# Optimization experiments

Hardware: AMD Instinct MI355X
Metric: run time of the kernel (lower is better)

The kernel has to match this reference:

```python
import jax, jax.numpy as jnp
import numpy as np

S, D, H, HD = 3072, 1280, 16, 80
FF = 4 * D
EPS = 1e-6


def layernorm(x, scale, bias):
    mu = jnp.mean(x, axis=-1, keepdims=True)
    var = jnp.mean(jnp.square(x - mu), axis=-1, keepdims=True)
    return (x - mu) * jax.lax.rsqrt(var + EPS) * scale + bias


def rotate_half(x):
    x1 = x[..., : x.shape[-1] // 2]
    x2 = x[..., x.shape[-1] // 2 :]
    return jnp.concatenate([-x2, x1], axis=-1)


def apply_rope(x, freqs):
    # x: (S,H,hd), freqs: (S,hd/2)
    cos = jnp.repeat(jnp.cos(freqs), 2, axis=-1)[:, None, :]  # (S,1,hd)
    sin = jnp.repeat(jnp.sin(freqs), 2, axis=-1)[:, None, :]
    return x * cos + rotate_half(x) * sin


def quick_gelu(x):
    return x * jax.nn.sigmoid(1.702 * x)


def setup_inputs() -> dict:
    key = jax.random.key(0)
    ks = jax.random.split(key, 12)
    s = 0.02
    return {
        "hidden_states": jax.random.normal(ks[0], (S, D), jnp.float32),
        "rotary_pos_emb": jax.random.normal(ks[1], (S, HD // 2), jnp.float32),
        "ln1_scale": jnp.ones((D,), jnp.float32),
        "ln1_bias": jnp.zeros((D,), jnp.float32),
        "ln2_scale": jnp.ones((D,), jnp.float32),
        "ln2_bias": jnp.zeros((D,), jnp.float32),
        "qkv_w": jax.random.normal(ks[2], (D, 3 * D), jnp.float32) * s,
        "qkv_b": jnp.zeros((3 * D,), jnp.float32),
        "proj_w": jax.random.normal(ks[3], (D, D), jnp.float32) * s,
        "proj_b": jnp.zeros((D,), jnp.float32),
        "fc1_w": jax.random.normal(ks[4], (D, FF), jnp.float32) * s,
        "fc1_b": jnp.zeros((FF,), jnp.float32),
        "fc2_w": jax.random.normal(ks[5], (FF, D), jnp.float32) * s,
        "fc2_b": jnp.zeros((D,), jnp.float32),
        "cu_seqlens": jnp.array([0, 1024, 2048, 3072], jnp.int32),
    }


def reference(hidden_states, rotary_pos_emb, ln1_scale, ln1_bias, ln2_scale,
              ln2_bias, qkv_w, qkv_b, proj_w, proj_b, fc1_w, fc1_b, fc2_w,
              fc2_b, cu_seqlens):
    x = hidden_states  # (S, D)
    h = layernorm(x, ln1_scale, ln1_bias)
    qkv = (h @ qkv_w + qkv_b).reshape(S, 3, H, HD)
    q, k, v = qkv[:, 0], qkv[:, 1], qkv[:, 2]  # each (S, H, hd)
    q = apply_rope(q, rotary_pos_emb)
    k = apply_rope(k, rotary_pos_emb)

    # block-diagonal varlen mask from cu_seqlens (same segment attends)
    ids = jnp.arange(S)
    seg = jnp.searchsorted(cu_seqlens, ids, side="right")  # (S,)
    valid = seg[:, None] == seg[None, :]  # (S, S)
    bias = jnp.where(valid, 0.0, jnp.finfo(q.dtype).min)

    scale = 1.0 / jnp.sqrt(jnp.asarray(HD, q.dtype))
    scores = jnp.einsum("qhd,khd->hqk", q, k) * scale + bias
    probs = jax.nn.softmax(scores.astype(jnp.float32), axis=-1).astype(q.dtype)
    attn = jnp.einsum("hqk,khd->qhd", probs, v).reshape(S, D)
    attn = attn @ proj_w + proj_b

    x = x + attn
    h2 = layernorm(x, ln2_scale, ln2_bias)
    mlp = quick_gelu(h2 @ fc1_w + fc1_b) @ fc2_w + fc2_b
    return x + mlp
```

## Files before the change

### kernel.cpp

```cpp
#include <hip/hip_runtime.h>

typedef __bf16 bf16x8 __attribute__((ext_vector_type(8)));
typedef float f32x4 __attribute__((ext_vector_type(4)));
typedef unsigned short u16;
typedef u16 u16x2 __attribute__((ext_vector_type(2)));
typedef u16 u16x4 __attribute__((ext_vector_type(4)));
typedef u16 u16x8 __attribute__((ext_vector_type(8)));
typedef float float4v __attribute__((ext_vector_type(4)));

__device__ __forceinline__ u16 f2bf(float f) {
    __bf16 b = (__bf16)f;
    return __builtin_bit_cast(unsigned short, b);
}
__device__ __forceinline__ float bf2f(u16 x) {
    __bf16 b = __builtin_bit_cast(__bf16, x);
    return (float)b;
}

__device__ __forceinline__ void gld16(const void* g, void* l) {
    __builtin_amdgcn_global_load_lds((const __attribute__((address_space(1))) void*)g,
                                     (__attribute__((address_space(3))) void*)l, 16, 0, 0);
}

__device__ __forceinline__ int xcd_swz(int orig, int nwg) {
    const int q = nwg >> 3, r = nwg & 7;
    const int xcd = orig & 7, pos = orig >> 3;
    return (xcd < r ? xcd * (q + 1) : r * (q + 1) + (xcd - r) * q) + pos;
}

__global__ __launch_bounds__(256) void transpose_all_kernel(
    const float* __restrict__ qkvw, const float* __restrict__ projw,
    const float* __restrict__ fc1w, const float* __restrict__ fc2w,
    u16* __restrict__ qkvwT, u16* __restrict__ projwT,
    u16* __restrict__ fc1wT, u16* __restrict__ fc2wT)
{
    __shared__ u16 tile[64][65];
    int bid = blockIdx.x;
    const float* W; u16* WT; int K, N, nx;
    if (bid < 1200)      { W = qkvw;  WT = qkvwT;  K = 1280; N = 3840; nx = 60; }
    else if (bid < 1600) { bid -= 1200; W = projw; WT = projwT; K = 1280; N = 1280; nx = 20; }
    else if (bid < 3200) { bid -= 1600; W = fc1w;  WT = fc1wT;  K = 1280; N = 5120; nx = 80; }
    else                 { bid -= 3200; W = fc2w;  WT = fc2wT;  K = 5120; N = 1280; nx = 20; }
    const int tx = threadIdx.x & 63, ty = threadIdx.x >> 6;
    const int n0 = (bid % nx) * 64, k0 = (bid / nx) * 64;
    #pragma unroll
    for (int i = ty; i < 64; i += 4)
        tile[i][tx] = f2bf(W[(size_t)(k0 + i) * N + n0 + tx]);
    __syncthreads();
    const int txh = threadIdx.x & 31, tyh = threadIdx.x >> 5;
    #pragma unroll
    for (int i = tyh; i < 64; i += 8) {
        u16x2 v2;
        v2[0] = tile[2 * txh][i];
        v2[1] = tile[2 * txh + 1][i];
        *reinterpret_cast<u16x2*>(&WT[(size_t)(n0 + i) * K + k0 + 2 * txh]) = v2;
    }
}

__global__ __launch_bounds__(256) void vtrans_kernel(
    const u16* __restrict__ qkv, u16* __restrict__ vt)
{
    __shared__ u16 tile[64][65];
    const int bs = blockIdx.x % 48, bd = blockIdx.x / 48;
    const int s0 = bs * 64, d0 = bd * 64;
    const int tx = threadIdx.x & 63, ty = threadIdx.x >> 6;
    #pragma unroll
    for (int i = ty; i < 64; i += 4)
        tile[i][tx] = qkv[(size_t)(s0 + i) * 3840 + 2560 + d0 + tx];
    __syncthreads();
    const int txh = threadIdx.x & 31, tyh = threadIdx.x >> 5;
    #pragma unroll
    for (int i = tyh; i < 64; i += 8) {
        u16x2 v2;
        v2[0] = tile[2 * txh][i];
        v2[1] = tile[2 * txh + 1][i];
        *reinterpret_cast<u16x2*>(&vt[(size_t)(d0 + i) * 3072 + s0 + 2 * txh]) = v2;
    }
}

__global__ __launch_bounds__(256) void ln_kernel(
    const float* __restrict__ x, const float* __restrict__ sc,
    const float* __restrict__ bias, u16* __restrict__ out)
{
    const int row = blockIdx.x, t = threadIdx.x;
    const float* xr = x + (size_t)row * 1280;
    float v[5], s1 = 0.f, s2 = 0.f;
    #pragma unroll
    for (int i = 0; i < 5; i++) {
        v[i] = xr[t + i * 256];
        s1 += v[i];
        s2 += v[i] * v[i];
    }
    #pragma unroll
    for (int off = 32; off; off >>= 1) {
        s1 += __shfl_down(s1, off);
        s2 += __shfl_down(s2, off);
    }
    __shared__ float rA[4], rB[4];
    if ((t & 63) == 0) { rA[t >> 6] = s1; rB[t >> 6] = s2; }
    __syncthreads();
    s1 = rA[0] + rA[1] + rA[2] + rA[3];
    s2 = rB[0] + rB[1] + rB[2] + rB[3];
    const float mu = s1 * (1.f / 1280.f);
    const float var = s2 * (1.f / 1280.f) - mu * mu;
    const float rstd = rsqrtf(var + 1e-6f);
    #pragma unroll
    for (int i = 0; i < 5; i++) {
        const int d = t + i * 256;
        out[(size_t)row * 1280 + d] = f2bf((v[i] - mu) * rstd * sc[d] + bias[d]);
    }
}

__global__ __launch_bounds__(256) void reduce4_ln_kernel(
    const u16* __restrict__ parts, const float* __restrict__ bias,
    const float* __restrict__ res, const float* __restrict__ lns,
    const float* __restrict__ lnb, float* __restrict__ xmid,
    u16* __restrict__ h2, size_t MN)
{
    const int row = blockIdx.x, t = threadIdx.x;
    float v[5], s1 = 0.f, s2 = 0.f;
    #pragma unroll
    for (int i = 0; i < 5; i++) {
        const int d = t + i * 256;
        const size_t idx = (size_t)row * 1280 + d;
        float a = bf2f(parts[idx]) + bf2f(parts[MN + idx])
                + bf2f(parts[2 * MN + idx]) + bf2f(parts[3 * MN + idx])
                + res[idx] + bias[d];
        v[i] = a;
        xmid[idx] = a;
        s1 += a;
        s2 += a * a;
    }
    #pragma unroll
    for (int off = 32; off; off >>= 1) {
        s1 += __shfl_down(s1, off);
        s2 += __shfl_down(s2, off);
    }
    __shared__ float rA[4], rB[4];
    if ((t & 63) == 0) { rA[t >> 6] = s1; rB[t >> 6] = s2; }
    __syncthreads();
    s1 = rA[0] + rA[1] + rA[2] + rA[3];
    s2 = rB[0] + rB[1] + rB[2] + rB[3];
    const float mu = s1 * (1.f / 1280.f);
    const float var = s2 * (1.f / 1280.f) - mu * mu;
    const float rstd = rsqrtf(var + 1e-6f);
    #pragma unroll
    for (int i = 0; i < 5; i++) {
        const int d = t + i * 256;
        h2[(size_t)row * 1280 + d] = f2bf((v[i] - mu) * rstd * lns[d] + lnb[d]);
    }
}

__global__ __launch_bounds__(256) void reduce4b_kernel(
    const u16* __restrict__ parts, const float* __restrict__ bias,
    const float* __restrict__ res, float* __restrict__ out, int N, size_t MN)
{
    const size_t i4 = ((size_t)blockIdx.x * 256 + threadIdx.x) * 4;
    if (i4 >= MN) return;
    float4v a = *reinterpret_cast<const float4v*>(res + i4);
    #pragma unroll
    for (int p = 0; p < 4; p++) {
        u16x4 v = *reinterpret_cast<const u16x4*>(parts + p * MN + i4);
        #pragma unroll
        for (int r = 0; r < 4; r++) a[r] += bf2f(v[r]);
    }
    const int col = (int)(i4 % N);
    a += *reinterpret_cast<const float4v*>(bias + col);
    *reinterpret_cast<float4v*>(out + i4) = a;
}

template <int GELU, int OUTB, int SPLIT>
__global__ __launch_bounds__(512, 2) void gemm256_kernel(
    const u16* __restrict__ A, const u16* __restrict__ BT,
    const float* __restrict__ bias,
    float* __restrict__ outF, u16* __restrict__ outB,
    int M, int N, int K)
{
    __shared__ u16 As[2][256 * 64];
    __shared__ u16 Bs[2][256 * 64];
    const int tid = threadIdx.x, lane = tid & 63, wave = tid >> 6;
    const int nwg = gridDim.x * gridDim.y;
    const int bid = xcd_swz(blockIdx.y * gridDim.x + blockIdx.x, nwg);
    const int m0 = (bid / gridDim.x) * 256, n0 = (bid % gridDim.x) * 256;
    const int wr = wave >> 2, wc = wave & 3;
    const int wm = wr * 128, wn = wc * 64;
    const int lr = lane & 15, lh = lane >> 4;
    const int xa = lr & 7;

    const int kchunk = K / SPLIT;
    const int kz = (SPLIT > 1) ? blockIdx.z : 0;
    const int kbeg = kz * kchunk;
    const int niter = kchunk >> 7;

    const int sr = lane >> 3;
    const int sc8 = (lane & 7) ^ sr;

    f32x4 acc[8][4] = {};
    bf16x8 bq[4][2];

    const char* aRd[2] = {
        (const char*)As + (wm + lr) * 128 + ((0 + lh) ^ xa) * 16,
        (const char*)As + (wm + lr) * 128 + ((4 + lh) ^ xa) * 16 };
    const char* bRd[2] = {
        (const char*)Bs + (wn + lr) * 128 + ((0 + lh) ^ xa) * 16,
        (const char*)Bs + (wn + lr) * 128 + ((4 + lh) ^ xa) * 16 };

    const u16 *aG[2][2], *bG[2][2];
    #pragma unroll
    for (int h = 0; h < 2; h++)
        #pragma unroll
        for (int j = 0; j < 2; j++) {
            const int row = h * 128 + j * 64 + wave * 8 + sr;
            aG[h][j] = A + (size_t)(m0 + row) * K + kbeg + sc8 * 8;
            bG[h][j] = BT + (size_t)(n0 + row) * K + kbeg + sc8 * 8;
        }

    auto stgA = [&](int t, int h) {
        u16* d = (u16*)As + (t & 1) * 16384 + h * 8192 + wave * 512;
        gld16(aG[h][0] + (size_t)t * 64, d);
        gld16(aG[h][1] + (size_t)t * 64, d + 4096);
    };
    auto stgB = [&](int t, int h) {
        u16* d = (u16*)Bs + (t & 1) * 16384 + h * 8192 + wave * 512;
        gld16(bG[h][0] + (size_t)t * 64, d);
        gld16(bG[h][1] + (size_t)t * 64, d + 4096);
    };

#define PHASE(BUF, Q, STGSTMT, WAITSTMT)                                        \
    {                                                                           \
        if ((Q) == 0) {                                                         \
            _Pragma("unroll") for (int ni = 0; ni < 4; ni++)                    \
                _Pragma("unroll") for (int kk = 0; kk < 2; kk++)                \
                    bq[ni][kk] = *reinterpret_cast<const bf16x8*>(              \
                        bRd[kk] + (BUF) * 32768 + ni * 2048);                   \
        }                                                                       \
        bf16x8 afq[2][2];                                                       \
        _Pragma("unroll") for (int m2 = 0; m2 < 2; m2++)                        \
            _Pragma("unroll") for (int kk = 0; kk < 2; kk++)                    \
                afq[m2][kk] = *reinterpret_cast<const bf16x8*>(                 \
                    aRd[kk] + (BUF) * 32768 + (Q) * 4096 + m2 * 2048);          \
        STGSTMT;                                                                \
        __builtin_amdgcn_s_barrier();                                           \
        asm volatile("s_waitcnt lgkmcnt(0)" ::: "memory");                      \
        __builtin_amdgcn_s_setprio(1);                                          \
        _Pragma("unroll") for (int kk = 0; kk < 2; kk++)                        \
            _Pragma("unroll") for (int m2 = 0; m2 < 2; m2++)                    \
                _Pragma("unroll") for (int ni = 0; ni < 4; ni++)                \
                    acc[(Q) * 2 + m2][ni] =                                     \
                        __builtin_amdgcn_mfma_f32_16x16x32_bf16(                \
                            afq[m2][kk], bq[ni][kk], acc[(Q) * 2 + m2][ni],     \
                            0, 0, 0);                                           \
        __builtin_amdgcn_s_setprio(0);                                          \
        WAITSTMT;                                                               \
        __builtin_amdgcn_s_barrier();                                           \
    }

    stgB(0, 0); stgB(0, 1);
    stgA(0, 0); stgA(0, 1);
    stgB(1, 0); stgB(1, 1);
    asm volatile("s_waitcnt vmcnt(4)" ::: "memory");
    __builtin_amdgcn_s_barrier();

    for (int i = 0; i < niter - 1; i++) {
        const int t0 = 2 * i, t1 = 2 * i + 1;
        PHASE(0, 0, stgA(t1, 0), (void)0);
        PHASE(0, 1, stgA(t1, 1), (void)0);
        PHASE(0, 2, stgB(t0 + 2, 0), (void)0);
        PHASE(0, 3, stgB(t0 + 2, 1),
              asm volatile("s_waitcnt vmcnt(4)" ::: "memory"));
        PHASE(1, 0, stgA(t0 + 2, 0), (void)0);
        PHASE(1, 1, stgA(t0 + 2, 1), (void)0);
        PHASE(1, 2, stgB(t1 + 2, 0), (void)0);
        PHASE(1, 3, stgB(t1 + 2, 1),
              asm volatile("s_waitcnt vmcnt(4)" ::: "memory"));
    }
    {
        const int t1 = 2 * niter - 1;
        PHASE(0, 0, stgA(t1, 0), (void)0);
        PHASE(0, 1, stgA(t1, 1), (void)0);
        PHASE(0, 2, (void)0, (void)0);
        PHASE(0, 3, (void)0,
              asm volatile("s_waitcnt vmcnt(0)" ::: "memory"));
        PHASE(1, 0, (void)0, (void)0);
        PHASE(1, 1, (void)0, (void)0);
        PHASE(1, 2, (void)0, (void)0);
        PHASE(1, 3, (void)0, (void)0);
    }
#undef PHASE

    if (SPLIT > 1) {
        u16* pf = outB + (size_t)kz * M * N;
        #pragma unroll
        for (int mi = 0; mi < 8; mi++)
            #pragma unroll
            for (int ni = 0; ni < 4; ni++) {
                const int col = n0 + wn + ni * 16 + lr;
                #pragma unroll
                for (int r = 0; r < 4; r++) {
                    const int rowg = m0 + wm + mi * 16 + lh * 4 + r;
                    pf[(size_t)rowg * N + col] = f2bf(acc[mi][ni][r]);
                }
            }
        return;
    }

    #pragma unroll
    for (int mi = 0; mi < 8; mi++) {
        #pragma unroll
        for (int ni = 0; ni < 4; ni++) {
            const int col = n0 + wn + ni * 16 + lr;
            const float bv = bias[col];
            #pragma unroll
            for (int r = 0; r < 4; r++) {
                const int rowg = m0 + wm + mi * 16 + lh * 4 + r;
                float v = acc[mi][ni][r] + bv;
                if (GELU) v = v * (1.0f / (1.0f + __expf(-1.702f * v)));
                if (OUTB) outB[(size_t)rowg * N + col] = f2bf(v);
            }
        }
    }
}

template <int SPLIT>
__global__ __launch_bounds__(256) void gemm_kernel(
    const u16* __restrict__ A, const u16* __restrict__ BT,
    u16* __restrict__ partB, int M, int N, int K)
{
    __shared__ u16 As[128 * 64];
    __shared__ u16 Bs[128 * 64];
    const int tid = threadIdx.x, lane = tid & 63, wave = tid >> 6;
    const int nwg = gridDim.x * gridDim.y;
    const int bid = xcd_swz(blockIdx.y * gridDim.x + blockIdx.x, nwg);
    const int m0 = (bid / gridDim.x) * 128, n0 = (bid % gridDim.x) * 128;
    const int wm = (wave >> 1) * 64, wn = (wave & 1) * 64;
    const int lr = lane & 15, lh = lane >> 4;
    const int xa = lr & 7;
    const int srow = lane >> 3;
    const int schunk = (lane & 7) ^ (srow & 7);

    const int kchunk = K / SPLIT;
    const int kz = (SPLIT > 1) ? blockIdx.z : 0;
    const int kbeg = kz * kchunk;

    const u16 *aG[4], *bG[4];
    u16 *dA[4], *dB[4];
    #pragma unroll
    for (int s = 0; s < 4; s++) {
        const int seg = wave + s * 4;
        const int row = seg * 8 + srow;
        aG[s] = A + (size_t)(m0 + row) * K + kbeg + schunk * 8;
        bG[s] = BT + (size_t)(n0 + row) * K + kbeg + schunk * 8;
        dA[s] = As + seg * 512;
        dB[s] = Bs + seg * 512;
    }
    const char* aRd[2] = {
        (const char*)As + (wm + lr) * 128 + ((0 + lh) ^ xa) * 16,
        (const char*)As + (wm + lr) * 128 + ((4 + lh) ^ xa) * 16 };
    const char* bRd[2] = {
        (const char*)Bs + (wn + lr) * 128 + ((0 + lh) ^ xa) * 16,
        (const char*)Bs + (wn + lr) * 128 + ((4 + lh) ^ xa) * 16 };

    f32x4 acc[4][4] = {};

    for (int ko = 0; ko < kchunk; ko += 64) {
        #pragma unroll
        for (int s = 0; s < 4; s++) {
            gld16(aG[s] + ko, dA[s]);
            gld16(bG[s] + ko, dB[s]);
        }
        asm volatile("s_waitcnt vmcnt(0)" ::: "memory");
        __syncthreads();

        bf16x8 af[4][2], bfr[4][2];
        #pragma unroll
        for (int mi = 0; mi < 4; mi++)
            #pragma unroll
            for (int kk = 0; kk < 2; kk++)
                af[mi][kk] = *reinterpret_cast<const bf16x8*>(aRd[kk] + mi * 2048);
        #pragma unroll
        for (int ni = 0; ni < 4; ni++)
            #pragma unroll
            for (int kk = 0; kk < 2; kk++)
                bfr[ni][kk] = *reinterpret_cast<const bf16x8*>(bRd[kk] + ni * 2048);
        #pragma unroll
        for (int kk = 0; kk < 2; kk++)
            #pragma unroll
            for (int mi = 0; mi < 4; mi++)
                #pragma unroll
                for (int ni = 0; ni < 4; ni++)
                    acc[mi][ni] = __builtin_amdgcn_mfma_f32_16x16x32_bf16(
                        af[mi][kk], bfr[ni][kk], acc[mi][ni], 0, 0, 0);
        __syncthreads();
    }

    u16* pf = partB + (size_t)kz * M * N;
    #pragma unroll
    for (int mi = 0; mi < 4; mi++)
        #pragma unroll
        for (int ni = 0; ni < 4; ni++) {
            const int col = n0 + wn + ni * 16 + lr;
            #pragma unroll
            for (int r = 0; r < 4; r++) {
                const int rowg = m0 + wm + mi * 16 + lh * 4 + r;
                pf[(size_t)rowg * N + col] = f2bf(acc[mi][ni][r]);
            }
        }
}

__global__ __launch_bounds__(256) void rope_kernel(
    const u16* __restrict__ qkv, const float* __restrict__ freqs,
    u16* __restrict__ qp, u16* __restrict__ kp)
{
    const int s = blockIdx.x, t = threadIdx.x;
    const float scale = 0.1118033988749895f;
    __shared__ float cs[40], sn[40];
    if (t < 40) {
        const float f = freqs[(size_t)s * 40 + t];
        cs[t] = cosf(f);
        sn[t] = sinf(f);
    }
    __syncthreads();
    const u16* row = qkv + (size_t)s * 3840;
    for (int i = t; i < 1280; i += 256) {
        const int h = i / 80, d = i % 80;
        const float c = cs[d >> 1], sv = sn[d >> 1];
        const float q0 = bf2f(row[i]);
        const float q1 = (d < 40) ? -bf2f(row[i + 40]) : bf2f(row[i - 40]);
        qp[((size_t)h * 3072 + s) * 96 + d] = f2bf((q0 * c + q1 * sv) * scale);
        const float k0 = bf2f(row[1280 + i]);
        const float k1 = (d < 40) ? -bf2f(row[1280 + i + 40]) : bf2f(row[1280 + i - 40]);
        kp[((size_t)h * 3072 + s) * 128 + d] = f2bf(k0 * c + k1 * sv);
    }
    {
        const int h = t / 16, d = 80 + (t % 16);
        qp[((size_t)h * 3072 + s) * 96 + d] = 0;
    }
    for (int i = t; i < 768; i += 256) {
        const int h = i / 48, d = 80 + (i % 48);
        kp[((size_t)h * 3072 + s) * 128 + d] = 0;
    }
}

__global__ __launch_bounds__(256) void attn_kernel(
    const u16* __restrict__ qp, const u16* __restrict__ kp,
    const u16* __restrict__ vt, u16* __restrict__ attn_out)
{
    const int tid = threadIdx.x, lane = tid & 63, wave = tid >> 6;
    const int w = xcd_swz(blockIdx.x, 768);
    const int qt = w & 15;
    const int h = (w >> 4) & 15;
    const int sq = w >> 8;
    const int lr = lane & 15, lh = lane >> 4;
    const int xa = lr & 7;
    const int qrow = sq * 1024 + qt * 64 + wave * 16;

    __shared__ u16 Ks[2][64 * 128];
    __shared__ u16 Vs[2][80 * 64];

    bf16x8 aq[3];
    {
        const u16* qb = qp + ((size_t)h * 3072 + qrow + lr) * 96 + lh * 8;
        #pragma unroll
        for (int d0 = 0; d0 < 3; d0++)
            aq[d0] = *reinterpret_cast<const bf16x8*>(qb + d0 * 32);
    }

    float m = -1e30f, l = 0.f;
    f32x4 acc[5] = {};

    const u16* kseg = kp + ((size_t)h * 3072 + sq * 1024) * 128;
    const u16* vseg = vt + (size_t)h * 80 * 3072 + sq * 1024;

    const int krow_l = lane >> 4;
    const int kch    = lane & 15;
    const int vrow_l = lane >> 3;
    const int vch    = lane & 7;

    const u16 *kG[4], *vG[3];
    u16 *kD[4], *vD[3];
    #pragma unroll
    for (int s = 0; s < 4; s++) {
        const int seg = wave + s * 4;
        const int row = seg * 4 + krow_l;
        kG[s] = kseg + (size_t)row * 128 + ((kch ^ (row & 7)) * 8);
        kD[s] = (u16*)Ks + seg * 512;
    }
    #pragma unroll
    for (int s = 0; s < 3; s++) {
        const int seg = wave + s * 4;
        const int row = (seg < 10) ? seg * 8 + vrow_l : 0;
        vG[s] = vseg + (size_t)row * 3072 + ((vch ^ (row & 7)) * 8);
        vD[s] = (u16*)Vs + seg * 512;
    }

    auto stageK = [&](int t, int buf) {
        #pragma unroll
        for (int s = 0; s < 4; s++)
            gld16(kG[s] + (size_t)t * 8192, kD[s] + buf * 8192);
    };
    auto stageV = [&](int t, int buf) {
        #pragma unroll
        for (int s = 0; s < 3; s++)
            if (wave + s * 4 < 10)
                gld16(vG[s] + t * 64, vD[s] + buf * 5120);
    };

    stageK(0, 0);
    stageV(0, 0);
    asm volatile("s_waitcnt vmcnt(0)" ::: "memory");
    __syncthreads();

    const char* kRd[3] = {
        (const char*)Ks + lr * 256 + ((0 + lh) ^ xa) * 16,
        (const char*)Ks + lr * 256 + ((4 + lh) ^ xa) * 16,
        (const char*)Ks + lr * 256 + ((8 + lh) ^ xa) * 16 };
    const char* vRd[2] = {
        (const char*)Vs + lr * 128 + ((0 + lh) ^ xa) * 16,
        (const char*)Vs + lr * 128 + ((4 + lh) ^ xa) * 16 };

    const int prow = wave * 16 + lr;
    const int psw = prow & 7;
    const char* pBase = (const char*)Ks + prow * 256;
    const int prd = ((12 + lh) ^ psw) << 4;

    for (int t = 0; t < 16; t++) {
        const int cur = t & 1;
        const int curK = cur * 16384, curV = cur * 10240;
        if (t < 15) {
            stageK(t + 1, cur ^ 1);
            stageV(t + 1, cur ^ 1);
        }

        f32x4 sc[4] = {};
        #pragma unroll
        for (int c = 0; c < 4; c++) {
            #pragma unroll
            for (int d0 = 0; d0 < 3; d0++) {
                bf16x8 kf = *reinterpret_cast<const bf16x8*>(kRd[d0] + curK + c * 4096);
                sc[c] = __builtin_amdgcn_mfma_f32_16x16x32_bf16(kf, aq[d0], sc[c], 0, 0, 0);
            }
        }

        float pmax = sc[0][0];
        #pragma unroll
        for (int c = 0; c < 4; c++)
            #pragma unroll
            for (int r = 0; r < 4; r++)
                pmax = fmaxf(pmax, sc[c][r]);
        pmax = fmaxf(pmax, __shfl_xor(pmax, 16));
        pmax = fmaxf(pmax, __shfl_xor(pmax, 32));

        if (!__all(pmax - m <= 8.0f)) {
            const float mn = fmaxf(m, pmax);
            const float fac = __expf(m - mn);
            m = mn;
            l *= fac;
            #pragma unroll
            for (int df = 0; df < 5; df++)
                #pragma unroll
                for (int r = 0; r < 4; r++)
                    acc[df][r] *= fac;
        }

        float p[4][4], rs = 0.f;
        #pragma unroll
        for (int c = 0; c < 4; c++)
            #pragma unroll
            for (int r = 0; r < 4; r++) {
                p[c][r] = __expf(sc[c][r] - m);
                rs += p[c][r];
            }
        rs += __shfl_xor(rs, 16);
        rs += __shfl_xor(rs, 32);
        l += rs;

        char* pb = (char*)pBase + curK;

        #pragma unroll
        for (int cc = 0; cc < 2; cc++) {
            u16x4 pw;
            #pragma unroll
            for (int r = 0; r < 4; r++)
                pw[r] = f2bf(p[cc][r]);
            *reinterpret_cast<u16x4*>(
                pb + (((12 + cc * 2 + (lh >> 1)) ^ psw) << 4) + (lh & 1) * 8) = pw;
        }
        asm volatile("s_waitcnt lgkmcnt(0)" ::: "memory");
        {
            bf16x8 pa = *reinterpret_cast<const bf16x8*>(pb + prd);
            asm volatile("s_waitcnt lgkmcnt(0)" ::: "memory");
            #pragma unroll
            for (int df = 0; df < 5; df++) {
                bf16x8 vf = *reinterpret_cast<const bf16x8*>(vRd[0] + curV + df * 2048);
                acc[df] = __builtin_amdgcn_mfma_f32_16x16x32_bf16(vf, pa, acc[df], 0, 0, 0);
            }
        }
        #pragma unroll
        for (int cc = 0; cc < 2; cc++) {
            u16x4 pw;
            #pragma unroll
            for (int r = 0; r < 4; r++)
                pw[r] = f2bf(p[2 + cc][r]);
            *reinterpret_cast<u16x4*>(
                pb + (((12 + cc * 2 + (lh >> 1)) ^ psw) << 4) + (lh & 1) * 8) = pw;
        }
        asm volatile("s_waitcnt lgkmcnt(0)" ::: "memory");
        {
            bf16x8 pa = *reinterpret_cast<const bf16x8*>(pb + prd);
            #pragma unroll
            for (int df = 0; df < 5; df++) {
                bf16x8 vf = *reinterpret_cast<const bf16x8*>(vRd[1] + curV + df * 2048);
                acc[df] = __builtin_amdgcn_mfma_f32_16x16x32_bf16(vf, pa, acc[df], 0, 0, 0);
            }
        }

        asm volatile("s_waitcnt vmcnt(0)" ::: "memory");
        __syncthreads();
    }

    const float invl = 1.0f / l;
    u16* orow = attn_out + (size_t)(qrow + lr) * 1280 + h * 80;
    #pragma unroll
    for (int df = 0; df < 5; df++) {
        u16x4 o;
        #pragma unroll
        for (int r = 0; r < 4; r++)
            o[r] = f2bf(acc[df][r] * invl);
        *reinterpret_cast<u16x4*>(orow + df * 16 + lh * 4) = o;
    }
}

extern "C" void kernel_launch(void* const* d_in, const int* in_sizes, int n_in,
                              void* d_out, int out_size, void* d_ws, size_t ws_size,
                              hipStream_t stream) {
    const float* hidden = (const float*)d_in[0];
    const float* rot    = (const float*)d_in[1];
    const float* ln1s   = (const float*)d_in[2];
    const float* ln1b   = (const float*)d_in[3];
    const float* ln2s   = (const float*)d_in[4];
    const float* ln2b   = (const float*)d_in[5];
    const float* qkvw   = (const float*)d_in[6];
    const float* qkvb   = (const float*)d_in[7];
    const float* projw  = (const float*)d_in[8];
    const float* projb  = (const float*)d_in[9];
    const float* fc1w   = (const float*)d_in[10];
    const float* fc1b   = (const float*)d_in[11];
    const float* fc2w   = (const float*)d_in[12];
    const float* fc2b   = (const float*)d_in[13];
    float* out = (float*)d_out;

    char* p = (char*)d_ws;
    auto alloc = [&](size_t n) { char* r = p; p += (n + 255) & ~(size_t)255; return r; };
    u16* qkvwT  = (u16*)alloc((size_t)3840 * 1280 * 2);
    u16* projwT = (u16*)alloc((size_t)1280 * 1280 * 2);
    u16* fc1wT  = (u16*)alloc((size_t)5120 * 1280 * 2);
    u16* fc2wT  = (u16*)alloc((size_t)1280 * 5120 * 2);
    u16* hbuf   = (u16*)alloc((size_t)3072 * 1280 * 2);
    u16* qkvbf  = (u16*)alloc((size_t)3072 * 5120 * 2);
    u16* attnb  = (u16*)alloc((size_t)3072 * 1280 * 2);
    float* xmid = (float*)alloc((size_t)3072 * 1280 * 4);
    u16* partsB = (u16*)alloc((size_t)4 * 3072 * 1280 * 2);
    u16* qp2 = partsB;
    u16* kp2 = qp2 + (size_t)16 * 3072 * 96;
    u16* vt2 = kp2 + (size_t)16 * 3072 * 128;
    u16* h2   = hbuf;
    u16* mlp1 = qkvbf;
    const size_t MN = (size_t)3072 * 1280;

    transpose_all_kernel<<<4800, 256, 0, stream>>>(
        qkvw, projw, fc1w, fc2w, qkvwT, projwT, fc1wT, fc2wT);

    ln_kernel<<<3072, 256, 0, stream>>>(hidden, ln1s, ln1b, hbuf);
    gemm256_kernel<0, 1, 1><<<dim3(15, 12), 512, 0, stream>>>(
        hbuf, qkvwT, qkvb, nullptr, qkvbf, 3072, 3840, 1280);
    rope_kernel<<<3072, 256, 0, stream>>>(qkvbf, rot, qp2, kp2);
    vtrans_kernel<<<960, 256, 0, stream>>>(qkvbf, vt2);
    attn_kernel<<<768, 256, 0, stream>>>(qp2, kp2, vt2, attnb);
    gemm_kernel<4><<<dim3(10, 24, 4), 256, 0, stream>>>(
        attnb, projwT, partsB, 3072, 1280, 1280);
    reduce4_ln_kernel<<<3072, 256, 0, stream>>>(
        partsB, projb, hidden, ln2s, ln2b, xmid, h2, MN);
    gemm256_kernel<1, 1, 1><<<dim3(20, 12), 512, 0, stream>>>(
        h2, fc1wT, fc1b, nullptr, mlp1, 3072, 5120, 1280);
    gemm256_kernel<0, 0, 4><<<dim3(5, 12, 4), 512, 0, stream>>>(
        mlp1, fc2wT, fc2b, nullptr, partsB, 3072, 1280, 5120);
    reduce4b_kernel<<<(int)(MN / 4 / 256), 256, 0, stream>>>(partsB, fc2b, xmid, out, 1280, MN);
}
```

Before: 263.2 us.

## Triple-buffer A tiles in gemm256 and store mid residual as bf16

The 256x256 GEMM now keeps three LDS buffers for A and two for B, with a rotating buffer schedule that prefetches two K-tiles ahead. It also replaces the runtime iteration count with a fully scheduled 20-tile loop, which assumes K equals 1280. The aim is to hide more global-load latency behind MFMA work, but the larger LDS footprint (160 KB) likely prevents two blocks per CU and lowers occupancy. Separately, the post-attention residual xmid is stored in bf16 instead of fp32 to cut memory traffic in the reduce kernels, at some cost in accuracy of the residual path.

Measured after the change: 266.1 us. No clear change (+1.1%).

```diff
diff --git a/kernel.cpp b/kernel.cpp
--- a/kernel.cpp
+++ b/kernel.cpp
@@ -114,7 +114,7 @@
 __global__ __launch_bounds__(256) void reduce4_ln_kernel(
     const u16* __restrict__ parts, const float* __restrict__ bias,
     const float* __restrict__ res, const float* __restrict__ lns,
-    const float* __restrict__ lnb, float* __restrict__ xmid,
+    const float* __restrict__ lnb, u16* __restrict__ xmid,
     u16* __restrict__ h2, size_t MN)
 {
     const int row = blockIdx.x, t = threadIdx.x;
@@ -127,7 +127,7 @@
                 + bf2f(parts[2 * MN + idx]) + bf2f(parts[3 * MN + idx])
                 + res[idx] + bias[d];
         v[i] = a;
-        xmid[idx] = a;
+        xmid[idx] = f2bf(a);
         s1 += a;
         s2 += a * a;
     }
@@ -153,11 +153,14 @@
 
 __global__ __launch_bounds__(256) void reduce4b_kernel(
     const u16* __restrict__ parts, const float* __restrict__ bias,
-    const float* __restrict__ res, float* __restrict__ out, int N, size_t MN)
+    const u16* __restrict__ res, float* __restrict__ out, int N, size_t MN)
 {
     const size_t i4 = ((size_t)blockIdx.x * 256 + threadIdx.x) * 4;
     if (i4 >= MN) return;
-    float4v a = *reinterpret_cast<const float4v*>(res + i4);
+    float4v a;
+    u16x4 rv = *reinterpret_cast<const u16x4*>(res + i4);
+    #pragma unroll
+    for (int r = 0; r < 4; r++) a[r] = bf2f(rv[r]);
     #pragma unroll
     for (int p = 0; p < 4; p++) {
         u16x4 v = *reinterpret_cast<const u16x4*>(parts + p * MN + i4);
@@ -176,7 +179,7 @@
     float* __restrict__ outF, u16* __restrict__ outB,
     int M, int N, int K)
 {
-    __shared__ u16 As[2][256 * 64];
+    __shared__ u16 As[3][256 * 64];
     __shared__ u16 Bs[2][256 * 64];
     const int tid = threadIdx.x, lane = tid & 63, wave = tid >> 6;
     const int nwg = gridDim.x * gridDim.y;
@@ -190,7 +193,6 @@
     const int kchunk = K / SPLIT;
     const int kz = (SPLIT > 1) ? blockIdx.z : 0;
     const int kbeg = kz * kchunk;
-    const int niter = kchunk >> 7;
 
     const int sr = lane >> 3;
     const int sc8 = (lane & 7) ^ sr;
@@ -198,12 +200,18 @@
     f32x4 acc[8][4] = {};
     bf16x8 bq[4][2];
 
-    const char* aRd[2] = {
-        (const char*)As + (wm + lr) * 128 + ((0 + lh) ^ xa) * 16,
-        (const char*)As + (wm + lr) * 128 + ((4 + lh) ^ xa) * 16 };
-    const char* bRd[2] = {
-        (const char*)Bs + (wn + lr) * 128 + ((0 + lh) ^ xa) * 16,
-        (const char*)Bs + (wn + lr) * 128 + ((4 + lh) ^ xa) * 16 };
+    const char* aRdB[3][2];
+    const char* bRdB[2][2];
+    #pragma unroll
+    for (int b = 0; b < 3; b++)
+        #pragma unroll
+        for (int kk = 0; kk < 2; kk++)
+            aRdB[b][kk] = (const char*)As[b] + (wm + lr) * 128 + ((kk * 4 + lh) ^ xa) * 16;
+    #pragma unroll
+    for (int b = 0; b < 2; b++)
+        #pragma unroll
+        for (int kk = 0; kk < 2; kk++)
+            bRdB[b][kk] = (const char*)Bs[b] + (wn + lr) * 128 + ((kk * 4 + lh) ^ xa) * 16;
 
     const u16 *aG[2][2], *bG[2][2];
     #pragma unroll
@@ -215,30 +223,30 @@
             bG[h][j] = BT + (size_t)(n0 + row) * K + kbeg + sc8 * 8;
         }
 
-    auto stgA = [&](int t, int h) {
-        u16* d = (u16*)As + (t & 1) * 16384 + h * 8192 + wave * 512;
+    auto stgA = [&](int t, int buf, int h) {
+        u16* d = (u16*)As + buf * 16384 + h * 8192 + wave * 512;
         gld16(aG[h][0] + (size_t)t * 64, d);
         gld16(aG[h][1] + (size_t)t * 64, d + 4096);
     };
-    auto stgB = [&](int t, int h) {
-        u16* d = (u16*)Bs + (t & 1) * 16384 + h * 8192 + wave * 512;
+    auto stgB = [&](int t, int buf, int h) {
+        u16* d = (u16*)Bs + buf * 16384 + h * 8192 + wave * 512;
         gld16(bG[h][0] + (size_t)t * 64, d);
         gld16(bG[h][1] + (size_t)t * 64, d + 4096);
     };
 
-#define PHASE(BUF, Q, STGSTMT, WAITSTMT)                                        \
+#define PH3(AB, BB, Q, RDB, STGSTMT, VMSTMT)                                    \
     {                                                                           \
-        if ((Q) == 0) {                                                         \
+        if (RDB) {                                                              \
             _Pragma("unroll") for (int ni = 0; ni < 4; ni++)                    \
                 _Pragma("unroll") for (int kk = 0; kk < 2; kk++)                \
                     bq[ni][kk] = *reinterpret_cast<const bf16x8*>(              \
-                        bRd[kk] + (BUF) * 32768 + ni * 2048);                   \
+                        bRdB[BB][kk] + ni * 2048);                              \
         }                                                                       \
         bf16x8 afq[2][2];                                                       \
         _Pragma("unroll") for (int m2 = 0; m2 < 2; m2++)                        \
             _Pragma("unroll") for (int kk = 0; kk < 2; kk++)                    \
                 afq[m2][kk] = *reinterpret_cast<const bf16x8*>(                 \
-                    aRd[kk] + (BUF) * 32768 + (Q) * 4096 + m2 * 2048);          \
+                    aRdB[AB][kk] + (Q) * 4096 + m2 * 2048);                     \
         STGSTMT;                                                                \
         __builtin_amdgcn_s_barrier();                                           \
         asm volatile("s_waitcnt lgkmcnt(0)" ::: "memory");                      \
@@ -251,42 +259,43 @@
                             afq[m2][kk], bq[ni][kk], acc[(Q) * 2 + m2][ni],     \
                             0, 0, 0);                                           \
         __builtin_amdgcn_s_setprio(0);                                          \
-        WAITSTMT;                                                               \
+        VMSTMT;                                                                 \
         __builtin_amdgcn_s_barrier();                                           \
     }
 
-    stgB(0, 0); stgB(0, 1);
-    stgA(0, 0); stgA(0, 1);
-    stgB(1, 0); stgB(1, 1);
-    asm volatile("s_waitcnt vmcnt(4)" ::: "memory");
+#define ITER3(T, AB, BB, A2)                                                    \
+    PH3(AB, BB, 0, 1, stgA((T) + 2, A2, 0), (void)0);                           \
+    PH3(AB, BB, 1, 0, stgA((T) + 2, A2, 1), (void)0);                           \
+    PH3(AB, BB, 2, 0, stgB((T) + 2, BB, 0), (void)0);                           \
+    PH3(AB, BB, 3, 0, stgB((T) + 2, BB, 1),                                     \
+        asm volatile("s_waitcnt vmcnt(8)" ::: "memory"));
+
+    stgA(0, 0, 0); stgA(0, 0, 1);
+    stgB(0, 0, 0); stgB(0, 0, 1);
+    stgA(1, 1, 0); stgA(1, 1, 1);
+    stgB(1, 1, 0); stgB(1, 1, 1);
+    asm volatile("s_waitcnt vmcnt(8)" ::: "memory");
     __builtin_amdgcn_s_barrier();
 
-    for (int i = 0; i < niter - 1; i++) {
-        const int t0 = 2 * i, t1 = 2 * i + 1;
-        PHASE(0, 0, stgA(t1, 0), (void)0);
-        PHASE(0, 1, stgA(t1, 1), (void)0);
-        PHASE(0, 2, stgB(t0 + 2, 0), (void)0);
-        PHASE(0, 3, stgB(t0 + 2, 1),
-              asm volatile("s_waitcnt vmcnt(4)" ::: "memory"));
-        PHASE(1, 0, stgA(t0 + 2, 0), (void)0);
-        PHASE(1, 1, stgA(t0 + 2, 1), (void)0);
-        PHASE(1, 2, stgB(t1 + 2, 0), (void)0);
-        PHASE(1, 3, stgB(t1 + 2, 1),
-              asm volatile("s_waitcnt vmcnt(4)" ::: "memory"));
-    }
-    {
-        const int t1 = 2 * niter - 1;
-        PHASE(0, 0, stgA(t1, 0), (void)0);
-        PHASE(0, 1, stgA(t1, 1), (void)0);
-        PHASE(0, 2, (void)0, (void)0);
-        PHASE(0, 3, (void)0,
-              asm volatile("s_waitcnt vmcnt(0)" ::: "memory"));
-        PHASE(1, 0, (void)0, (void)0);
-        PHASE(1, 1, (void)0, (void)0);
-        PHASE(1, 2, (void)0, (void)0);
-        PHASE(1, 3, (void)0, (void)0);
-    }
-#undef PHASE
+    for (int tt = 0; tt < 3; tt++) {
+        const int tb = 6 * tt;
+        ITER3(tb + 0, 0, 0, 2);
+        ITER3(tb + 1, 1, 1, 0);
+        ITER3(tb + 2, 2, 0, 1);
+        ITER3(tb + 3, 0, 1, 2);
+        ITER3(tb + 4, 1, 0, 0);
+        ITER3(tb + 5, 2, 1, 1);
+    }
+    PH3(0, 0, 0, 1, (void)0, (void)0);
+    PH3(0, 0, 1, 0, (void)0, (void)0);
+    PH3(0, 0, 2, 0, (void)0, (void)0);
+    PH3(0, 0, 3, 0, (void)0, asm volatile("s_waitcnt vmcnt(0)" ::: "memory"));
+    PH3(1, 1, 0, 1, (void)0, (void)0);
+    PH3(1, 1, 1, 0, (void)0, (void)0);
+    PH3(1, 1, 2, 0, (void)0, (void)0);
+    PH3(1, 1, 3, 0, (void)0, (void)0);
+#undef ITER3
+#undef PH3
 
     if (SPLIT > 1) {
         u16* pf = outB + (size_t)kz * M * N;
@@ -658,7 +667,7 @@
     u16* hbuf   = (u16*)alloc((size_t)3072 * 1280 * 2);
     u16* qkvbf  = (u16*)alloc((size_t)3072 * 5120 * 2);
     u16* attnb  = (u16*)alloc((size_t)3072 * 1280 * 2);
-    float* xmid = (float*)alloc((size_t)3072 * 1280 * 4);
+    u16* xmid   = (u16*)alloc((size_t)3072 * 1280 * 2);
     u16* partsB = (u16*)alloc((size_t)4 * 3072 * 1280 * 2);
     u16* qp2 = partsB;
     u16* kp2 = qp2 + (size_t)16 * 3072 * 96;
```
